# Performance work log

Hardware: AMD Instinct MI355X
Metric: run time of the kernel (lower is better)

The kernel has to match this reference:

```python
import jax, jax.numpy as jnp
import numpy as np

N_HEAD = 16

def setup_inputs() -> dict:
    key = jax.random.key(0)
    k1, k2, k3 = jax.random.split(key, 3)
    B, T, C = 4, 2048, 1024
    x = jax.random.normal(k1, (B, T, C), dtype=jnp.float32)
    w_qkv = jax.random.normal(k2, (C, 3 * C), dtype=jnp.float32) * (1.0 / np.sqrt(C))
    w_proj = jax.random.normal(k3, (C, C), dtype=jnp.float32) * (1.0 / np.sqrt(C))
    return {"x": x, "w_qkv": w_qkv, "w_proj": w_proj}

def reference(x, w_qkv, w_proj):
    B, T, C = x.shape
    H = N_HEAD
    D = C // H
    qkv = x @ w_qkv                      # [B,T,3C]
    q, k, v = jnp.split(qkv, 3, axis=-1)
    # [B,T,C] -> [B,H,T,D]
    q = q.reshape(B, T, H, D).transpose(0, 2, 1, 3)
    k = k.reshape(B, T, H, D).transpose(0, 2, 1, 3)
    v = v.reshape(B, T, H, D).transpose(0, 2, 1, 3)
    scale = 1.0 / np.sqrt(D).astype(np.float32)
    att = jnp.einsum('bhqd,bhkd->bhqk', q, k) * scale   # [B,H,T,T]
    causal = jnp.tril(jnp.ones((T, T), dtype=bool))
    att = jnp.where(causal[None, None], att, jnp.finfo(att.dtype).min)
    att = jax.nn.softmax(att, axis=-1)
    y = jnp.einsum('bhqk,bhkd->bhqd', att, v)           # [B,H,T,D]
    y = y.transpose(0, 2, 1, 3).reshape(B, T, C)
    return y @ w_proj
```

## Files before the change

kernel.cpp:

```cpp
#include <hip/hip_runtime.h>
#include <hip/hip_bf16.h>


typedef unsigned short us;
typedef short bf16x8 __attribute__((ext_vector_type(8)));
typedef float f32x4 __attribute__((ext_vector_type(4)));
typedef unsigned short us8 __attribute__((ext_vector_type(8)));

extern "C" __device__ float __ocml_native_exp2_f32(float);

__device__ __forceinline__ us f2bf(float f) {
  union { float f; unsigned u; } v; v.f = f;
  unsigned r = v.u + 0x7fff + ((v.u >> 16) & 1);
  return (us)(r >> 16);
}
__device__ __forceinline__ us f2bf_hw(float f) {
  __hip_bfloat16 h = __float2bfloat16(f);
  return *reinterpret_cast<us*>(&h);
}

__device__ __forceinline__ void gload_lds16(const us* g, us* l) {
  __builtin_amdgcn_global_load_lds(
      (const __attribute__((address_space(1))) void*)g,
      (__attribute__((address_space(3))) void*)l, 16, 0, 0);
}

__global__ __launch_bounds__(256) void k_cvt(const float* __restrict__ in,
                                             us* __restrict__ out, int n) {
  int i = (blockIdx.x * blockDim.x + threadIdx.x) * 4;
  if (i >= n) return;
  float4 v = *reinterpret_cast<const float4*>(in + i);
  ushort4 o;
  o.x = f2bf(v.x); o.y = f2bf(v.y); o.z = f2bf(v.z); o.w = f2bf(v.w);
  *reinterpret_cast<ushort4*>(out + i) = o;
}

__global__ __launch_bounds__(256) void k_tc(const float* __restrict__ in,
                                            us* __restrict__ out, int R, int C) {
  __shared__ float tile[32][33];
  int c0 = blockIdx.x * 32, r0 = blockIdx.y * 32;
  int tx = threadIdx.x, ty = threadIdx.y;
  for (int j = 0; j < 32; j += 8)
    tile[ty + j][tx] = in[(size_t)(r0 + ty + j) * C + c0 + tx];
  __syncthreads();
  for (int j = 0; j < 32; j += 8)
    out[(size_t)(c0 + ty + j) * R + r0 + tx] = f2bf(tile[tx][ty + j]);
}

template<int EPI>
__global__ __launch_bounds__(256) void k_gemm(
    const us* __restrict__ A, const us* __restrict__ Bt,
    float* __restrict__ Cf,
    us* __restrict__ Qb, us* __restrict__ Kb, us* __restrict__ Vt,
    int M, int N, int K)
{
  __shared__ us As[128][64];
  __shared__ us Bs[128][64];
  int t = threadIdx.x;
  int lane = t & 63, w = t >> 6;
  int wm = (w >> 1) * 64, wn = (w & 1) * 64;
  int fr = lane & 15, fq = lane >> 4;
  int m0 = blockIdx.y * 128, n0 = blockIdx.x * 128;
  int srow = lane >> 3, scol = (lane & 7) * 8;
  f32x4 acc[4][4] = {};
  for (int k0 = 0; k0 < K; k0 += 64) {
    __syncthreads();
    for (int p = 0; p < 4; ++p) {
      int row = w * 32 + p * 8;
      gload_lds16(&A[(size_t)(m0 + row + srow) * K + k0 + scol], &As[row][0]);
      gload_lds16(&Bt[(size_t)(n0 + row + srow) * K + k0 + scol], &Bs[row][0]);
    }
    __syncthreads();
    for (int kk = 0; kk < 64; kk += 32) {
      bf16x8 a[4], b[4];
      for (int mi = 0; mi < 4; ++mi)
        a[mi] = *reinterpret_cast<const bf16x8*>(&As[wm + mi * 16 + fr][kk + fq * 8]);
      for (int ni = 0; ni < 4; ++ni)
        b[ni] = *reinterpret_cast<const bf16x8*>(&Bs[wn + ni * 16 + fr][kk + fq * 8]);
      for (int mi = 0; mi < 4; ++mi)
        for (int ni = 0; ni < 4; ++ni)
          acc[mi][ni] = __builtin_amdgcn_mfma_f32_16x16x32_bf16(a[mi], b[ni], acc[mi][ni], 0, 0, 0);
    }
  }
  for (int mi = 0; mi < 4; ++mi) for (int ni = 0; ni < 4; ++ni) {
    int n  = n0 + wn + ni * 16 + fr;
    int mb = m0 + wm + mi * 16 + fq * 4;
    if (EPI == 0) {
      for (int r = 0; r < 4; ++r)
        Cf[(size_t)(mb + r) * N + n] = acc[mi][ni][r];
    } else {
      int s = n >> 10, c = n & 1023, h = c >> 6, d = c & 63;
      for (int r = 0; r < 4; ++r) {
        int mm = mb + r; int b = mm >> 11, tt = mm & 2047;
        float v = acc[mi][ni][r];
        size_t qk = ((size_t)((b << 4) + h) * 2048 + tt) * 64 + d;
        if (s == 0)      Qb[qk] = f2bf(v * 0.1803368801111244f);
        else if (s == 1) Kb[qk] = f2bf(v);
        else Vt[((size_t)((b << 4) + h) * 64 + d) * 2048 + tt] = f2bf(v);
      }
    }
  }
}

__global__ __launch_bounds__(512) void k_attn(
    const us* __restrict__ Q, const us* __restrict__ Kv, const us* __restrict__ Vt,
    us* __restrict__ O)
{
  __shared__ us K_lds[64][72];
  __shared__ us V_lds[64][72];
  __shared__ us P_lds[8][16][72];
  int t = threadIdx.x;
  int lane = t & 63, w = t >> 6;
  int fr = lane & 15, fq = lane >> 4;
  int bh = blockIdx.y, px = blockIdx.x;
  const size_t hb = (size_t)bh * 2048 * 64;
  int sr = t >> 3, sc = (t & 7) * 8;
  int b = bh >> 4, h = bh & 15;

  for (int sidx = 0; sidx < 2; ++sidx) {
    int qblk = sidx ? (15 - px) : px;
    int q0 = qblk * 128 + w * 16;

    bf16x8 qf[2];
    qf[0] = *reinterpret_cast<const bf16x8*>(&Q[hb + (size_t)(q0 + fr) * 64 + fq * 8]);
    qf[1] = *reinterpret_cast<const bf16x8*>(&Q[hb + (size_t)(q0 + fr) * 64 + 32 + fq * 8]);

    f32x4 o[4] = {};
    float m_run[4] = {-1e30f, -1e30f, -1e30f, -1e30f};
    float s_run[4] = {};
    int nt = 2 * qblk + 2;
    for (int it = 0; it < nt; ++it) {
      int kv0 = it * 64;
      __syncthreads();
      *reinterpret_cast<us8*>(&K_lds[sr][sc]) =
          *reinterpret_cast<const us8*>(&Kv[hb + (size_t)(kv0 + sr) * 64 + sc]);
      *reinterpret_cast<us8*>(&V_lds[sr][sc]) =
          *reinterpret_cast<const us8*>(&Vt[hb + (size_t)sr * 2048 + kv0 + sc]);
      __syncthreads();

      if (kv0 > q0 + 15) continue;

      f32x4 s[4] = {};
      for (int c = 0; c < 2; ++c)
        for (int ni = 0; ni < 4; ++ni) {
          bf16x8 kf = *reinterpret_cast<const bf16x8*>(&K_lds[ni * 16 + fr][c * 32 + fq * 8]);
          s[ni] = __builtin_amdgcn_mfma_f32_16x16x32_bf16(qf[c], kf, s[ni], 0, 0, 0);
        }

      if (kv0 + 64 > q0) {
        for (int ni = 0; ni < 4; ++ni)
          for (int r = 0; r < 4; ++r)
            if (kv0 + ni * 16 + fr > q0 + fq * 4 + r) s[ni][r] = -1e30f;
      }

      float pmax[4];
      for (int r = 0; r < 4; ++r)
        pmax[r] = fmaxf(fmaxf(s[0][r], s[1][r]), fmaxf(s[2][r], s[3][r]));
      for (int msk = 1; msk < 16; msk <<= 1)
        for (int r = 0; r < 4; ++r)
          pmax[r] = fmaxf(pmax[r], __shfl_xor(pmax[r], msk, 64));

      float scl[4];
      for (int r = 0; r < 4; ++r) {
        float mn = fmaxf(m_run[r], pmax[r]);
        scl[r] = __ocml_native_exp2_f32(m_run[r] - mn);
        m_run[r] = mn;
      }
      float pv[4][4], psum[4] = {};
      for (int ni = 0; ni < 4; ++ni)
        for (int r = 0; r < 4; ++r) {
          pv[ni][r] = __ocml_native_exp2_f32(s[ni][r] - m_run[r]);
          psum[r] += pv[ni][r];
        }
      for (int msk = 1; msk < 16; msk <<= 1)
        for (int r = 0; r < 4; ++r)
          psum[r] += __shfl_xor(psum[r], msk, 64);
      for (int r = 0; r < 4; ++r) s_run[r] = s_run[r] * scl[r] + psum[r];
      for (int df = 0; df < 4; ++df)
        for (int r = 0; r < 4; ++r) o[df][r] *= scl[r];

      for (int ni = 0; ni < 4; ++ni)
        for (int r = 0; r < 4; ++r)
          P_lds[w][fq * 4 + r][ni * 16 + fr] = f2bf_hw(pv[ni][r]);
      asm volatile("s_waitcnt lgkmcnt(0)" ::: "memory");

      for (int c = 0; c < 2; ++c) {
        bf16x8 pa = *reinterpret_cast<const bf16x8*>(&P_lds[w][fr][c * 32 + fq * 8]);
        for (int df = 0; df < 4; ++df) {
          bf16x8 vf = *reinterpret_cast<const bf16x8*>(&V_lds[df * 16 + fr][c * 32 + fq * 8]);
          o[df] = __builtin_amdgcn_mfma_f32_16x16x32_bf16(pa, vf, o[df], 0, 0, 0);
        }
      }
    }

    for (int df = 0; df < 4; ++df)
      for (int r = 0; r < 4; ++r) {
        int tt = q0 + fq * 4 + r;
        float val = o[df][r] / s_run[r];
        O[(size_t)(b * 2048 + tt) * 1024 + h * 64 + df * 16 + fr] = f2bf_hw(val);
      }
  }
}

extern "C" void kernel_launch(void* const* d_in, const int* in_sizes, int n_in,
                              void* d_out, int out_size, void* d_ws, size_t ws_size,
                              hipStream_t stream) {
  (void)in_sizes; (void)n_in; (void)out_size; (void)ws_size;
  const float* x      = (const float*)d_in[0];
  const float* w_qkv  = (const float*)d_in[1];
  const float* w_proj = (const float*)d_in[2];
  float* out = (float*)d_out;

  us* xb     = (us*)d_ws;
  us* wqkvT  = xb     + 8388608;
  us* wprojT = wqkvT  + 3145728;
  us* Qb     = wprojT + 1048576;
  us* Kb     = Qb     + 8388608;
  us* Vtb    = Kb     + 8388608;
  us* attn   = Vtb    + 8388608;

  k_cvt<<<8192, 256, 0, stream>>>(x, xb, 8388608);
  k_tc<<<dim3(96, 32), dim3(32, 8), 0, stream>>>(w_qkv, wqkvT, 1024, 3072);
  k_tc<<<dim3(32, 32), dim3(32, 8), 0, stream>>>(w_proj, wprojT, 1024, 1024);
  k_gemm<1><<<dim3(24, 64), 256, 0, stream>>>(xb, wqkvT, nullptr, Qb, Kb, Vtb, 8192, 3072, 1024);
  k_attn<<<dim3(8, 64), 512, 0, stream>>>(Qb, Kb, Vtb, attn);
  k_gemm<0><<<dim3(8, 64), 256, 0, stream>>>(attn, wprojT, out, nullptr, nullptr, nullptr, 8192, 1024, 1024);
}
```

Before: 344.4 us.

## Prefetch K/V tiles into registers, swizzle LDS, lazy softmax rescale, remap blocks

The attention kernel now loads the next K/V tile into registers while the current tile is being computed, so global-load latency overlaps the MFMA work. The K/V LDS tiles drop their padding and use an XOR swizzle to avoid bank conflicts. The online-softmax rescale is skipped unless some row max grows by more than 8 in log2 units, which saves exp and multiply work but allows exponentials up to 2^8 in the accumulators. Block indices are remapped so that heads are grouped per XCD, to improve L2 locality.

```diff
diff --git a/kernel.cpp b/kernel.cpp
--- a/kernel.cpp
+++ b/kernel.cpp
@@ -106,15 +106,21 @@
     const us* __restrict__ Q, const us* __restrict__ Kv, const us* __restrict__ Vt,
     us* __restrict__ O)
 {
-  __shared__ us K_lds[64][72];
-  __shared__ us V_lds[64][72];
+  __shared__ us K_lds[64][64];
+  __shared__ us V_lds[64][64];
   __shared__ us P_lds[8][16][72];
   int t = threadIdx.x;
   int lane = t & 63, w = t >> 6;
   int fr = lane & 15, fq = lane >> 4;
-  int bh = blockIdx.y, px = blockIdx.x;
+  int flat = blockIdx.y * 8 + blockIdx.x;
+  int xcd = flat & 7, idx = flat >> 3;
+  int bh = (idx & 7) | (xcd << 3);
+  int px = idx >> 3;
   const size_t hb = (size_t)bh * 2048 * 64;
-  int sr = t >> 3, sc = (t & 7) * 8;
+  int sr = t >> 3;
+  int ss = t & 7;
+  int ssw = (ss ^ (sr & 7)) * 8;
+  int fr7 = fr & 7;
   int b = bh >> 4, h = bh & 15;
 
   for (int sidx = 0; sidx < 2; ++sidx) {
@@ -129,13 +135,20 @@
     float m_run[4] = {-1e30f, -1e30f, -1e30f, -1e30f};
     float s_run[4] = {};
     int nt = 2 * qblk + 2;
+
+    us8 kreg = *reinterpret_cast<const us8*>(&Kv[hb + (size_t)sr * 64 + ss * 8]);
+    us8 vreg = *reinterpret_cast<const us8*>(&Vt[hb + (size_t)sr * 2048 + ss * 8]);
+
     for (int it = 0; it < nt; ++it) {
       int kv0 = it * 64;
       __syncthreads();
-      *reinterpret_cast<us8*>(&K_lds[sr][sc]) =
-          *reinterpret_cast<const us8*>(&Kv[hb + (size_t)(kv0 + sr) * 64 + sc]);
-      *reinterpret_cast<us8*>(&V_lds[sr][sc]) =
-          *reinterpret_cast<const us8*>(&Vt[hb + (size_t)sr * 2048 + kv0 + sc]);
+      *reinterpret_cast<us8*>(&K_lds[sr][ssw]) = kreg;
+      *reinterpret_cast<us8*>(&V_lds[sr][ssw]) = vreg;
+      if (it + 1 < nt) {
+        int kn = kv0 + 64;
+        kreg = *reinterpret_cast<const us8*>(&Kv[hb + (size_t)(kn + sr) * 64 + ss * 8]);
+        vreg = *reinterpret_cast<const us8*>(&Vt[hb + (size_t)sr * 2048 + kn + ss * 8]);
+      }
       __syncthreads();
 
       if (kv0 > q0 + 15) continue;
@@ -143,7 +156,8 @@
       f32x4 s[4] = {};
       for (int c = 0; c < 2; ++c)
         for (int ni = 0; ni < 4; ++ni) {
-          bf16x8 kf = *reinterpret_cast<const bf16x8*>(&K_lds[ni * 16 + fr][c * 32 + fq * 8]);
+          int sl = (((c << 2) | fq) ^ fr7) * 8;
+          bf16x8 kf = *reinterpret_cast<const bf16x8*>(&K_lds[ni * 16 + fr][sl]);
           s[ni] = __builtin_amdgcn_mfma_f32_16x16x32_bf16(qf[c], kf, s[ni], 0, 0, 0);
         }
 
@@ -160,12 +174,18 @@
         for (int r = 0; r < 4; ++r)
           pmax[r] = fmaxf(pmax[r], __shfl_xor(pmax[r], msk, 64));
 
-      float scl[4];
-      for (int r = 0; r < 4; ++r) {
-        float mn = fmaxf(m_run[r], pmax[r]);
-        scl[r] = __ocml_native_exp2_f32(m_run[r] - mn);
-        m_run[r] = mn;
-      }
+      float worst = fmaxf(fmaxf(pmax[0] - m_run[0], pmax[1] - m_run[1]),
+                          fmaxf(pmax[2] - m_run[2], pmax[3] - m_run[3]));
+      if (__any(worst > 8.0f)) {
+        for (int r = 0; r < 4; ++r) {
+          float mn = fmaxf(m_run[r], pmax[r]);
+          float scl = __ocml_native_exp2_f32(m_run[r] - mn);
+          m_run[r] = mn;
+          s_run[r] *= scl;
+          for (int df = 0; df < 4; ++df) o[df][r] *= scl;
+        }
+      }
+
       float pv[4][4], psum[4] = {};
       for (int ni = 0; ni < 4; ++ni)
         for (int r = 0; r < 4; ++r) {
@@ -175,9 +195,7 @@
       for (int msk = 1; msk < 16; msk <<= 1)
         for (int r = 0; r < 4; ++r)
           psum[r] += __shfl_xor(psum[r], msk, 64);
-      for (int r = 0; r < 4; ++r) s_run[r] = s_run[r] * scl[r] + psum[r];
-      for (int df = 0; df < 4; ++df)
-        for (int r = 0; r < 4; ++r) o[df][r] *= scl[r];
+      for (int r = 0; r < 4; ++r) s_run[r] += psum[r];
 
       for (int ni = 0; ni < 4; ++ni)
         for (int r = 0; r < 4; ++r)
@@ -187,7 +205,8 @@
       for (int c = 0; c < 2; ++c) {
         bf16x8 pa = *reinterpret_cast<const bf16x8*>(&P_lds[w][fr][c * 32 + fq * 8]);
         for (int df = 0; df < 4; ++df) {
-          bf16x8 vf = *reinterpret_cast<const bf16x8*>(&V_lds[df * 16 + fr][c * 32 + fq * 8]);
+          int sl = (((c << 2) | fq) ^ fr7) * 8;
+          bf16x8 vf = *reinterpret_cast<const bf16x8*>(&V_lds[df * 16 + fr][sl]);
           o[df] = __builtin_amdgcn_mfma_f32_16x16x32_bf16(pa, vf, o[df], 0, 0, 0);
         }
       }
```

Result: faster. 323.5 us (-6.1%).
